# Kernel optimization log

Hardware: AMD Instinct MI355X
Metric: run time of the kernel (lower is better)

## Reference

```python
import jax, jax.numpy as jnp
import numpy as np

# static config (matches init_kwargs)
B, H, W, C = 8, 64, 64, 512
HEADS, WS, SHIFT = 16, 8, 4
N = WS * WS
HIDDEN = 4 * C
HEAD_DIM = C // HEADS
SCALE = HEAD_DIM ** -0.5
EPS = 1e-3  # keras LayerNormalization default epsilon


def _rel_pos_index(ws):
    # replicates tf.meshgrid default 'xy' indexing used in the source
    coords = np.stack(np.meshgrid(np.arange(ws), np.arange(ws)))  # [2, ws, ws]
    cf = coords.reshape(2, -1)
    rel = (cf[:, :, None] - cf[:, None, :]).transpose(1, 2, 0)  # [N, N, 2]
    rel[:, :, 0] += ws - 1
    rel[:, :, 1] += ws - 1
    rel[:, :, 0] *= 2 * ws - 1
    return jnp.asarray(rel.sum(-1))  # [N, N] int


def _attn_mask(h, w, ws, shift):
    img = np.zeros((h, w), dtype=np.float32)
    cnt = 0
    for hs in (slice(0, -ws), slice(-ws, -shift), slice(-shift, None)):
        for wsl in (slice(0, -ws), slice(-ws, -shift), slice(-shift, None)):
            img[hs, wsl] = cnt
            cnt += 1
    mw = img.reshape(h // ws, ws, w // ws, ws).transpose(0, 2, 1, 3).reshape(-1, ws * ws)  # [nW, N]
    diff = mw[:, None, :] - mw[:, :, None]
    return jnp.asarray(np.where(diff != 0, -100.0, 0.0).astype(np.float32))  # [nW, N, N]


REL_IDX = _rel_pos_index(WS)
ATTN_MASK = _attn_mask(H, W, WS, SHIFT)
NW = (H // WS) * (W // WS)


def _ln(x, g, b):
    mu = jnp.mean(x, -1, keepdims=True)
    var = jnp.mean(jnp.square(x - mu), -1, keepdims=True)
    return (x - mu) * jax.lax.rsqrt(var + EPS) * g + b


def setup_inputs() -> dict:
    key = jax.random.key(0)
    ks = jax.random.split(key, 14)
    s = 0.02
    return {
        "x": jax.random.normal(ks[0], (B, H * W, C), jnp.float32),
        "norm1_g": jnp.ones((C,), jnp.float32),
        "norm1_b": jnp.zeros((C,), jnp.float32),
        "qkv_w": jax.random.normal(ks[1], (C, 3 * C), jnp.float32) * s,
        "qkv_b": jnp.zeros((3 * C,), jnp.float32),
        "rpb_table": jax.random.normal(ks[2], ((2 * WS - 1) ** 2, HEADS), jnp.float32) * s,
        "proj_w": jax.random.normal(ks[3], (C, C), jnp.float32) * s,
        "proj_b": jnp.zeros((C,), jnp.float32),
        "norm2_g": jnp.ones((C,), jnp.float32),
        "norm2_b": jnp.zeros((C,), jnp.float32),
        "fc1_w": jax.random.normal(ks[4], (C, HIDDEN), jnp.float32) * s,
        "fc1_b": jnp.zeros((HIDDEN,), jnp.float32),
        "fc2_w": jax.random.normal(ks[5], (HIDDEN, C), jnp.float32) * s,
        "fc2_b": jnp.zeros((C,), jnp.float32),
    }


def reference(x, norm1_g, norm1_b, qkv_w, qkv_b, rpb_table, proj_w, proj_b,
              norm2_g, norm2_b, fc1_w, fc1_b, fc2_w, fc2_b):
    shortcut = x
    h = _ln(x, norm1_g, norm1_b).reshape(B, H, W, C)
    # cyclic shift (SW-MSA)
    h = jnp.roll(h, (-SHIFT, -SHIFT), axis=(1, 2))
    # window partition -> (B*nW, N, C)
    h = h.reshape(B, H // WS, WS, W // WS, WS, C).transpose(0, 1, 3, 2, 4, 5)
    h = h.reshape(B * NW, N, C)
    # qkv
    qkv = (h @ qkv_w + qkv_b).reshape(B * NW, N, 3, HEADS, HEAD_DIM).transpose(2, 0, 3, 1, 4)
    q, k, v = qkv[0] * SCALE, qkv[1], qkv[2]  # each [Bw, heads, N, hd]
    attn = jnp.einsum('bhnd,bhmd->bhnm', q, k)  # [Bw, heads, N, N]
    bias = rpb_table[REL_IDX.reshape(-1)].reshape(N, N, HEADS).transpose(2, 0, 1)
    attn = attn + bias[None]
    # shifted-window mask, per source: mask add -> softmax -> softmax AGAIN (source quirk)
    attn = attn.reshape(B, NW, HEADS, N, N) + ATTN_MASK[None, :, None]
    attn = attn.reshape(B * NW, HEADS, N, N)
    attn = jax.nn.softmax(attn, axis=-1)
    attn = jax.nn.softmax(attn, axis=-1)
    o = jnp.einsum('bhnm,bhmd->bhnd', attn, v).transpose(0, 2, 1, 3).reshape(B * NW, N, C)
    o = o @ proj_w + proj_b
    # window reverse + reverse shift
    o = o.reshape(B, H // WS, W // WS, WS, WS, C).transpose(0, 1, 3, 2, 4, 5).reshape(B, H, W, C)
    o = jnp.roll(o, (SHIFT, SHIFT), axis=(1, 2)).reshape(B, H * W, C)
    x = shortcut + o
    # MLP: source applies gelu twice (Dense activation + explicit gelu)
    y = _ln(x, norm2_g, norm2_b)
    y = jax.nn.gelu(jax.nn.gelu(y @ fc1_w + fc1_b, approximate=False), approximate=False)
    y = y @ fc2_w + fc2_b
    return x + y
```

## Files before the change

kernel.cpp:

```cpp
#include <hip/hip_runtime.h>
#include <hip/hip_bf16.h>
#include <math.h>


typedef unsigned short ushort_t;
typedef __attribute__((ext_vector_type(8))) short short8;
typedef __attribute__((ext_vector_type(8))) __bf16 bf16x8;
typedef __attribute__((ext_vector_type(4))) float f32x4;

#define DEVINL __device__ __forceinline__

DEVINL float bf2f(ushort_t u){ union {unsigned int i; float f;} c; c.i = ((unsigned)u)<<16; return c.f; }
DEVINL ushort_t f2bf(float f){ union {unsigned int i; float f;} c; c.f = f; unsigned r = c.i + 0x7fffu + ((c.i>>16)&1u); return (ushort_t)(r>>16); }

typedef const __attribute__((address_space(1))) void* gas_t;
typedef __attribute__((address_space(3))) void* las_t;
DEVINL void load_lds16(const void* g, void* l) {
  __builtin_amdgcn_global_load_lds((gas_t)g, (las_t)l, 16, 0, 0);
}

DEVINL float gelu_fast(float v){
  float z  = fabsf(v) * 0.70710678118654752f;
  float t  = __builtin_amdgcn_rcpf(fmaf(0.47047f, z, 1.0f));
  float p  = t * fmaf(t, fmaf(t, 0.7478556f, -0.0958798f), 0.3480242f);
  float e  = __expf(-z*z);
  float er = fmaf(-p, e, 1.0f);
  float hs = (v >= 0.f) ? 0.5f : -0.5f;
  return v * fmaf(hs, er, 0.5f);
}

DEVINL int win_map_row(int t){
  int bw = t >> 6, n = t & 63;
  int b  = bw >> 6, wdx = bw & 63;
  int wh = wdx >> 3, ww = wdx & 7;
  int r  = n >> 3,  c  = n & 7;
  int hh = (wh*8 + r + 4) & 63;
  int w2 = (ww*8 + c + 4) & 63;
  return (b << 12) + (hh << 6) + w2;
}

DEVINL void remap_mn(int bid, int nwg, int nbn, int BM, int BN, int& m0, int& n0){
  int q    = nwg >> 3;
  int lbid = (bid & 7)*q + (bid >> 3);
  m0 = (lbid / nbn) * BM;
  n0 = (lbid % nbn) * BN;
}

__global__ void transpose_all(const float* __restrict__ qkv_w, const float* __restrict__ proj_w,
                              const float* __restrict__ fc1_w, const float* __restrict__ fc2_w,
                              ushort_t* __restrict__ wqT, ushort_t* __restrict__ wpT,
                              ushort_t* __restrict__ w1T, ushort_t* __restrict__ w2T){
  __shared__ float t[32][33];
  int bid = blockIdx.x;
  const float* in; ushort_t* out; int R, Ccols, bx, by;
  if (bid < 768)      { in=qkv_w;  out=wqT; R=512;  Ccols=1536; bx=(bid%48)*32;        by=(bid/48)*32; }
  else if (bid < 1024){ int b=bid-768;  in=proj_w; out=wpT; R=512;  Ccols=512;  bx=(b%16)*32; by=(b/16)*32; }
  else if (bid < 2048){ int b=bid-1024; in=fc1_w;  out=w1T; R=512;  Ccols=2048; bx=(b%64)*32; by=(b/64)*32; }
  else                { int b=bid-2048; in=fc2_w;  out=w2T; R=2048; Ccols=512;  bx=(b%16)*32; by=(b/16)*32; }
  int x = threadIdx.x, y = threadIdx.y;
  #pragma unroll
  for (int i=0;i<32;i+=8) t[y+i][x] = in[(size_t)(by+y+i)*Ccols + bx + x];
  __syncthreads();
  #pragma unroll
  for (int i=0;i<32;i+=8) out[(size_t)(bx+y+i)*R + by + x] = f2bf(t[x][y+i]);
}

__global__ __launch_bounds__(256) void ln_kernel(const float* __restrict__ in,
    const float* __restrict__ g, const float* __restrict__ bta,
    ushort_t* __restrict__ out, int windowed){
  int tid = threadIdx.x; int l = tid & 63; int w = tid >> 6;
  int t = blockIdx.x * 4 + w;
  int src = windowed ? win_map_row(t) : t;
  const float* row = in + (size_t)src * 512;
  float4 v0 = *(const float4*)(row + l*8);
  float4 v1 = *(const float4*)(row + l*8 + 4);
  float f[8] = {v0.x,v0.y,v0.z,v0.w, v1.x,v1.y,v1.z,v1.w};
  float s=0.f, s2=0.f;
  #pragma unroll
  for (int j=0;j<8;j++){ s += f[j]; s2 += f[j]*f[j]; }
  #pragma unroll
  for (int m=1;m<64;m<<=1){ s += __shfl_xor(s,m); s2 += __shfl_xor(s2,m); }
  float mu  = s * (1.f/512.f);
  float var = s2*(1.f/512.f) - mu*mu;
  float rs  = rsqrtf(var + 1e-3f);
  float4 g0 = *(const float4*)(g + l*8),   g1 = *(const float4*)(g + l*8 + 4);
  float4 b0 = *(const float4*)(bta + l*8), b1 = *(const float4*)(bta + l*8 + 4);
  float gg[8] = {g0.x,g0.y,g0.z,g0.w, g1.x,g1.y,g1.z,g1.w};
  float bb[8] = {b0.x,b0.y,b0.z,b0.w, b1.x,b1.y,b1.z,b1.w};
  short8 o;
  #pragma unroll
  for (int j=0;j<8;j++) o[j] = (short)f2bf((f[j]-mu)*rs*gg[j] + bb[j]);
  *(short8*)(out + (size_t)t*512 + l*8) = o;
}

template<int EPI>
__global__ __launch_bounds__(512, 4) void gemmv(
    const ushort_t* __restrict__ A, const ushort_t* __restrict__ Bt,
    const float* __restrict__ bias, void* __restrict__ Cout_v,
    const float* __restrict__ xres, int M, int N, int K, int nbn)
{
  __shared__ ushort_t lds[24576];
  __shared__ float2 g2tab[(EPI==1)?1024:1];
  const int tid = threadIdx.x; const int l = tid & 63; const int w = tid >> 6;
  const int wm = w >> 1, wn = w & 1;
  int m0, n0; remap_mn(blockIdx.x, gridDim.x, nbn, 256, 128, m0, n0);
  const int lr = l & 15, lk = l >> 4;
  const int nt = K >> 5;

  if (EPI == 1){
    #pragma unroll
    for (int i=0;i<2;i++){
      int idx = tid*2 + i;
      float vi = -4.f + (float)idx*(1.f/128.f);
      float a  = gelu_fast(gelu_fast(vi));
      float b  = gelu_fast(gelu_fast(vi + (1.f/128.f)));
      g2tab[idx] = make_float2(a, b - a);
    }
  }

  const int r0 = tid >> 2;
  const int kc = ((tid & 3) - (r0 >> 1)) & 3;
  const size_t aG = (size_t)(m0 + r0) * K + kc*8;
  const size_t bG = (size_t)(n0 + r0) * K + kc*8;

  #define STAGE_T(tt, LB) do { \
    load_lds16(A  + aG +                  (size_t)(tt)*32, &lds[(LB) +        w*512]); \
    load_lds16(A  + aG + 128*(size_t)K +  (size_t)(tt)*32, &lds[(LB) + 4096 + w*512]); \
    load_lds16(Bt + bG +                  (size_t)(tt)*32, &lds[(LB) + 8192 + w*512]); \
  } while(0)

  int aoff[4], boff[4];
  #pragma unroll
  for (int mf=0; mf<4; mf++){
    int row = wm*64 + mf*16 + lr;
    aoff[mf] = (row*4 + ((lk + (row>>1)) & 3))*8;
  }
  #pragma unroll
  for (int nf=0; nf<4; nf++){
    int row = wn*64 + nf*16 + lr;
    boff[nf] = 8192 + (row*4 + ((lk + (row>>1)) & 3))*8;
  }

  f32x4 acc[4][4] = {};

  STAGE_T(0, 0);
  STAGE_T(1, 12288);
  asm volatile("s_waitcnt vmcnt(3)" ::: "memory");
  __builtin_amdgcn_s_barrier();

  for (int t = 0; t < nt; ++t){
    const int Lb = (t & 1) ? 12288 : 0;
    const int t2 = (t+2 < nt) ? t+2 : nt-1;
    bf16x8 af[4], bfr[4];
    #pragma unroll
    for (int mf=0; mf<4; mf++) af[mf]  = *(const bf16x8*)&lds[Lb + aoff[mf]];
    #pragma unroll
    for (int nf=0; nf<4; nf++) bfr[nf] = *(const bf16x8*)&lds[Lb + boff[nf]];
    __builtin_amdgcn_sched_barrier(0);
    asm volatile("s_waitcnt lgkmcnt(0)" ::: "memory");
    __builtin_amdgcn_s_barrier();
    __builtin_amdgcn_sched_barrier(0);
    STAGE_T(t2, Lb);
    __builtin_amdgcn_sched_barrier(0);
    __builtin_amdgcn_s_setprio(1);
    #pragma unroll
    for (int mf=0; mf<4; mf++)
      #pragma unroll
      for (int nf=0; nf<4; nf++)
        acc[mf][nf] = __builtin_amdgcn_mfma_f32_16x16x32_bf16(af[mf], bfr[nf], acc[mf][nf], 0,0,0);
    __builtin_amdgcn_s_setprio(0);
    __builtin_amdgcn_sched_barrier(0);
    asm volatile("s_waitcnt vmcnt(3)" ::: "memory");
    __builtin_amdgcn_s_barrier();
  }

  asm volatile("s_waitcnt vmcnt(0)" ::: "memory");
  __builtin_amdgcn_s_barrier();
  __builtin_amdgcn_sched_barrier(0);

  int erow = l >> 2, ecc = l & 3;
  if (EPI == 0 || EPI == 1){
    ushort_t* tw = lds + w*1152;
    #pragma unroll
    for (int mf=0; mf<4; mf++){
      #pragma unroll
      for (int nf=0; nf<4; nf++){
        float bz = bias[n0 + wn*64 + nf*16 + lr];
        #pragma unroll
        for (int rg=0; rg<4; rg++){
          float v = acc[mf][nf][rg] + bz;
          if (EPI == 1){
            float u  = fminf(fmaxf((v + 4.f)*128.f, 0.f), 1023.999f);
            int   iu = (int)u;
            float fr = u - (float)iu;
            float2 pq = g2tab[iu];
            float rr = fmaf(fr, pq.y, pq.x);
            rr = (v >  4.f) ? v   : rr;
            v  = (v < -4.f) ? 0.f : rr;
          }
          tw[(lk*4+rg)*72 + nf*16 + lr] = f2bf(v);
        }
      }
      short8 p0 = *(const short8*)(tw + erow*72 + ecc*16);
      short8 p1 = *(const short8*)(tw + erow*72 + ecc*16 + 8);
      int grow = m0 + wm*64 + mf*16 + erow;
      int col  = n0 + wn*64 + ecc*16;
      *(short8*)&((ushort_t*)Cout_v)[(size_t)grow*N + col]     = p0;
      *(short8*)&((ushort_t*)Cout_v)[(size_t)grow*N + col + 8] = p1;
    }
  } else {
    float* twf = (float*)lds + w*1152;
    #pragma unroll
    for (int mf=0; mf<4; mf++){
      #pragma unroll
      for (int nf=0; nf<4; nf++){
        float bz = bias[n0 + wn*64 + nf*16 + lr];
        #pragma unroll
        for (int rg=0; rg<4; rg++)
          twf[(lk*4+rg)*72 + nf*16 + lr] = acc[mf][nf][rg] + bz;
      }
      int grow = m0 + wm*64 + mf*16 + erow;
      int col  = n0 + wn*64 + ecc*16;
      float4 q0 = *(const float4*)(twf + erow*72 + ecc*16);
      float4 q1 = *(const float4*)(twf + erow*72 + ecc*16 + 4);
      float4 q2 = *(const float4*)(twf + erow*72 + ecc*16 + 8);
      float4 q3 = *(const float4*)(twf + erow*72 + ecc*16 + 12);
      size_t off;
      float* o = (float*)Cout_v;
      if (EPI == 2){
        int row2 = win_map_row(grow);
        off = (size_t)row2*512 + col;
        float4 x0 = *(const float4*)(xres + off);
        float4 x1 = *(const float4*)(xres + off + 4);
        float4 x2 = *(const float4*)(xres + off + 8);
        float4 x3 = *(const float4*)(xres + off + 12);
        q0 = make_float4(q0.x+x0.x, q0.y+x0.y, q0.z+x0.z, q0.w+x0.w);
        q1 = make_float4(q1.x+x1.x, q1.y+x1.y, q1.z+x1.z, q1.w+x1.w);
        q2 = make_float4(q2.x+x2.x, q2.y+x2.y, q2.z+x2.z, q2.w+x2.w);
        q3 = make_float4(q3.x+x3.x, q3.y+x3.y, q3.z+x3.z, q3.w+x3.w);
      } else {
        off = (size_t)grow*N + col;
        float4 x0 = *(const float4*)(o + off);
        float4 x1 = *(const float4*)(o + off + 4);
        float4 x2 = *(const float4*)(o + off + 8);
        float4 x3 = *(const float4*)(o + off + 12);
        q0 = make_float4(q0.x+x0.x, q0.y+x0.y, q0.z+x0.z, q0.w+x0.w);
        q1 = make_float4(q1.x+x1.x, q1.y+x1.y, q1.z+x1.z, q1.w+x1.w);
        q2 = make_float4(q2.x+x2.x, q2.y+x2.y, q2.z+x2.z, q2.w+x2.w);
        q3 = make_float4(q3.x+x3.x, q3.y+x3.y, q3.z+x3.z, q3.w+x3.w);
      }
      *(float4*)(o + off)      = q0;
      *(float4*)(o + off + 4)  = q1;
      *(float4*)(o + off + 8)  = q2;
      *(float4*)(o + off + 12) = q3;
    }
  }
  #undef STAGE_T
}

DEVINL int band3(int t){ return (t<56) ? 0 : ((t<60) ? 1 : 2); }

union frag_u { short8 s; bf16x8 b; };

__global__ __launch_bounds__(256) void attn_kernel(const ushort_t* __restrict__ qkv,
    const float* __restrict__ rpb, ushort_t* __restrict__ o)
{
  __shared__ ushort_t sP[4][64*64];
  __shared__ ushort_t sV[4][64*32];
  int tid = threadIdx.x; int l = tid & 63; int w = tid >> 6;
  int p = blockIdx.x*4 + w;
  int bw = p >> 4, head = p & 15;
  int lr = l & 15, lk = l >> 4;
  const ushort_t* base = qkv + (size_t)bw*64*1536 + head*32;

  #pragma unroll
  for (int c=0;c<4;c++){
    int idx = c*64 + l;
    int row = idx >> 2, cc = idx & 3;
    load_lds16(base + 1024 + (size_t)row*1536 + cc*8, &sV[w][0] + c*512);
  }

  bf16x8 qf[4], kf[4];
  #pragma unroll
  for (int m=0;m<4;m++) qf[m] = *(const bf16x8*)(base +       (size_t)(m*16+lr)*1536 + lk*8);
  #pragma unroll
  for (int m=0;m<4;m++) kf[m] = *(const bf16x8*)(base + 512 + (size_t)(m*16+lr)*1536 + lk*8);

  f32x4 s[4][4] = {};
  #pragma unroll
  for (int m=0;m<4;m++)
    #pragma unroll
    for (int n=0;n<4;n++)
      s[m][n] = __builtin_amdgcn_mfma_f32_16x16x32_bf16(qf[m], kf[n], s[m][n], 0,0,0);

  int wdx = bw & 63; int wh = wdx >> 3, ww = wdx & 7;
  const float SCALE = 0.17677669529663687f;
  #pragma unroll
  for (int m=0;m<4;m++){
    #pragma unroll
    for (int r=0;r<4;r++){
      int i  = m*16 + lk*4 + r;
      int ri = band3(wh*8 + (i>>3))*3 + band3(ww*8 + (i&7));
      int ix = i & 7, iy = i >> 3;
      #pragma unroll
      for (int n=0;n<4;n++){
        int j   = n*16 + lr;
        int rj  = band3(wh*8 + (j>>3))*3 + band3(ww*8 + (j&7));
        int idx = 15*(ix - (j&7) + 7) + (iy - (j>>3) + 7);
        float bv = rpb[idx*16 + head];
        float mk = (ri == rj) ? 0.f : -100.f;
        s[m][n][r] = s[m][n][r]*SCALE + bv + mk;
      }
    }
  }

  #pragma unroll
  for (int pass=0; pass<2; pass++){
    #pragma unroll
    for (int m=0;m<4;m++){
      #pragma unroll
      for (int r=0;r<4;r++){
        float mx = fmaxf(fmaxf(s[m][0][r], s[m][1][r]), fmaxf(s[m][2][r], s[m][3][r]));
        #pragma unroll
        for (int d=1;d<16;d<<=1) mx = fmaxf(mx, __shfl_xor(mx, d));
        float sum = 0.f;
        #pragma unroll
        for (int n=0;n<4;n++){ float e = __expf(s[m][n][r]-mx); s[m][n][r]=e; sum += e; }
        #pragma unroll
        for (int d=1;d<16;d<<=1) sum += __shfl_xor(sum, d);
        float inv = 1.f/sum;
        #pragma unroll
        for (int n=0;n<4;n++) s[m][n][r] = s[m][n][r]*inv;
      }
    }
  }

  ushort_t* pl = &sP[w][0];
  #pragma unroll
  for (int m=0;m<4;m++)
    #pragma unroll
    for (int r=0;r<4;r++){
      int i = m*16 + lk*4 + r;
      #pragma unroll
      for (int n=0;n<4;n++){
        int j = n*16 + lr;
        int byte = i*128 + ((j*2) ^ ((i&7)<<4));
        pl[byte>>1] = f2bf(s[m][n][r]);
      }
    }

  asm volatile("s_waitcnt vmcnt(0)" ::: "memory");
  const ushort_t* vl = &sV[w][0];
  frag_u vf[2][2];
  #pragma unroll
  for (int kb=0;kb<2;kb++)
    #pragma unroll
    for (int nb=0;nb<2;nb++){
      #pragma unroll
      for (int j=0;j<8;j++){
        int k = kb*32 + lk*8 + j;
        vf[kb][nb].s[j] = (short)vl[k*32 + nb*16 + lr];
      }
    }

  f32x4 oacc[4][2] = {};
  #pragma unroll
  for (int m=0;m<4;m++){
    #pragma unroll
    for (int kb=0;kb<2;kb++){
      int row  = m*16 + lr;
      int byte = row*128 + ((kb*64 + lk*16) ^ ((row&7)<<4));
      bf16x8 pf = *(const bf16x8*)(pl + (byte>>1));
      #pragma unroll
      for (int nb=0;nb<2;nb++)
        oacc[m][nb] = __builtin_amdgcn_mfma_f32_16x16x32_bf16(pf, vf[kb][nb].b, oacc[m][nb], 0,0,0);
    }
  }

  ushort_t* orow = o + (size_t)bw*64*512 + head*32;
  #pragma unroll
  for (int m=0;m<4;m++)
    #pragma unroll
    for (int nb=0;nb<2;nb++)
      #pragma unroll
      for (int r=0;r<4;r++){
        int i = m*16 + lk*4 + r;
        int d = nb*16 + lr;
        orow[(size_t)i*512 + d] = f2bf(oacc[m][nb][r]);
      }
}

extern "C" void kernel_launch(void* const* d_in, const int* in_sizes, int n_in,
                              void* d_out, int out_size, void* d_ws, size_t ws_size,
                              hipStream_t stream) {
  const float* x      = (const float*)d_in[0];
  const float* n1g    = (const float*)d_in[1];
  const float* n1b    = (const float*)d_in[2];
  const float* qkv_w  = (const float*)d_in[3];
  const float* qkv_b  = (const float*)d_in[4];
  const float* rpb    = (const float*)d_in[5];
  const float* proj_w = (const float*)d_in[6];
  const float* proj_b = (const float*)d_in[7];
  const float* n2g    = (const float*)d_in[8];
  const float* n2b    = (const float*)d_in[9];
  const float* fc1_w  = (const float*)d_in[10];
  const float* fc1_b  = (const float*)d_in[11];
  const float* fc2_w  = (const float*)d_in[12];
  const float* fc2_b  = (const float*)d_in[13];
  float* out = (float*)d_out;

  ushort_t* ws = (ushort_t*)d_ws;
  size_t off = 0;
  ushort_t* wqT = ws + off; off += (size_t)1536*512;
  ushort_t* wpT = ws + off; off += (size_t)512*512;
  ushort_t* w1T = ws + off; off += (size_t)2048*512;
  ushort_t* w2T = ws + off; off += (size_t)512*2048;
  ushort_t* R1  = ws + off; off += (size_t)32768*512;
  ushort_t* R2  = ws + off; off += (size_t)32768*2048;
  if (ws_size < off*sizeof(ushort_t)) return;

  transpose_all<<<3072, dim3(32,8), 0, stream>>>(qkv_w, proj_w, fc1_w, fc2_w, wqT, wpT, w1T, w2T);

  ln_kernel<<<8192, 256, 0, stream>>>(x, n1g, n1b, R1, 1);
  gemmv<0><<<1536, 512, 0, stream>>>(R1, wqT, qkv_b, R2, nullptr, 32768, 1536, 512, 12);
  attn_kernel<<<2048, 256, 0, stream>>>(R2, rpb, R1);
  gemmv<2><<<512, 512, 0, stream>>>(R1, wpT, proj_b, out, x, 32768, 512, 512, 4);
  ln_kernel<<<8192, 256, 0, stream>>>(out, n2g, n2b, R1, 0);
  gemmv<1><<<2048, 512, 0, stream>>>(R1, w1T, fc1_b, R2, nullptr, 32768, 2048, 512, 16);
  gemmv<3><<<512, 512, 0, stream>>>(R2, w2T, fc2_b, out, nullptr, 32768, 512, 2048, 4);
}
```

Before: 407.4 us.

## Add 256x256-tile GEMM with BK=64 phased pipeline for QKV, proj, fc2

Adds a gemm256 kernel using 256x256 output tiles, a K-step of 64, 64KB LDS double buffering and a four-phase schedule that interleaves A/B staging with MFMA groups. QKV, projection and fc2 GEMMs now use it, which raises arithmetic intensity and halves the tile count. The fc1 GEMM keeps the old kernel, but its double-GELU table changes from interpolated 1024 entries to nearest-lookup 2048 entries, trading accuracy for fewer epilogue ops. The larger tile cuts occupancy to 2 blocks per CU and leaves only 256 blocks for the N=512 GEMMs, which may underfill the GPU.

```diff
diff --git a/kernel.cpp b/kernel.cpp
--- a/kernel.cpp
+++ b/kernel.cpp
@@ -9,6 +9,8 @@
 typedef __attribute__((ext_vector_type(4))) float f32x4;
 
 #define DEVINL __device__ __forceinline__
+
+union frag_u { short8 s; bf16x8 b; };
 
 DEVINL float bf2f(ushort_t u){ union {unsigned int i; float f;} c; c.i = ((unsigned)u)<<16; return c.f; }
 DEVINL ushort_t f2bf(float f){ union {unsigned int i; float f;} c; c.f = f; unsigned r = c.i + 0x7fffu + ((c.i>>16)&1u); return (ushort_t)(r>>16); }
@@ -93,117 +95,118 @@
   *(short8*)(out + (size_t)t*512 + l*8) = o;
 }
 
+#define G_STAGE(G, base, h, tt, LB) do { \
+    load_lds16((G) + (base) + (size_t)((h)*128)*K    + (size_t)(tt)*64, &lds[(LB) + (h)*8192 +        w*512]); \
+    load_lds16((G) + (base) + (size_t)((h)*128+64)*K + (size_t)(tt)*64, &lds[(LB) + (h)*8192 + 4096 + w*512]); \
+  } while(0)
+
+#define NOWAIT
+#define VM4 asm volatile("s_waitcnt vmcnt(4)" ::: "memory")
+
+#define PHASE(mp, STAGE_STMT, EXTRA) do { \
+    bf16x8 a0 = *(const bf16x8*)&lds[ALb + aoff[2*(mp)  ][0]]; \
+    bf16x8 a1 = *(const bf16x8*)&lds[ALb + aoff[2*(mp)  ][1]]; \
+    bf16x8 a2 = *(const bf16x8*)&lds[ALb + aoff[2*(mp)+1][0]]; \
+    bf16x8 a3 = *(const bf16x8*)&lds[ALb + aoff[2*(mp)+1][1]]; \
+    STAGE_STMT; \
+    EXTRA; \
+    __builtin_amdgcn_s_barrier(); \
+    asm volatile("s_waitcnt lgkmcnt(0)" ::: "memory"); \
+    __builtin_amdgcn_sched_barrier(0); \
+    __builtin_amdgcn_s_setprio(1); \
+    _Pragma("unroll") \
+    for (int nf=0; nf<4; nf++){ \
+      acc[2*(mp)  ][nf] = __builtin_amdgcn_mfma_f32_16x16x32_bf16(a0, bfr[nf][0], acc[2*(mp)  ][nf], 0,0,0); \
+      acc[2*(mp)  ][nf] = __builtin_amdgcn_mfma_f32_16x16x32_bf16(a1, bfr[nf][1], acc[2*(mp)  ][nf], 0,0,0); \
+      acc[2*(mp)+1][nf] = __builtin_amdgcn_mfma_f32_16x16x32_bf16(a2, bfr[nf][0], acc[2*(mp)+1][nf], 0,0,0); \
+      acc[2*(mp)+1][nf] = __builtin_amdgcn_mfma_f32_16x16x32_bf16(a3, bfr[nf][1], acc[2*(mp)+1][nf], 0,0,0); \
+    } \
+    __builtin_amdgcn_s_setprio(0); \
+    __builtin_amdgcn_sched_barrier(0); \
+    __builtin_amdgcn_s_barrier(); \
+  } while(0)
+
 template<int EPI>
-__global__ __launch_bounds__(512, 4) void gemmv(
+__global__ __launch_bounds__(512, 2) void gemm256(
     const ushort_t* __restrict__ A, const ushort_t* __restrict__ Bt,
     const float* __restrict__ bias, void* __restrict__ Cout_v,
     const float* __restrict__ xres, int M, int N, int K, int nbn)
 {
-  __shared__ ushort_t lds[24576];
-  __shared__ float2 g2tab[(EPI==1)?1024:1];
+  __shared__ ushort_t lds[65536];
   const int tid = threadIdx.x; const int l = tid & 63; const int w = tid >> 6;
-  const int wm = w >> 1, wn = w & 1;
-  int m0, n0; remap_mn(blockIdx.x, gridDim.x, nbn, 256, 128, m0, n0);
+  const int wm = w >> 2, wn = w & 3;
+  int m0, n0;
+  remap_mn(blockIdx.x, gridDim.x, nbn, 256, 256, m0, n0);
   const int lr = l & 15, lk = l >> 4;
-  const int nt = K >> 5;
-
-  if (EPI == 1){
-    #pragma unroll
-    for (int i=0;i<2;i++){
-      int idx = tid*2 + i;
-      float vi = -4.f + (float)idx*(1.f/128.f);
-      float a  = gelu_fast(gelu_fast(vi));
-      float b  = gelu_fast(gelu_fast(vi + (1.f/128.f)));
-      g2tab[idx] = make_float2(a, b - a);
-    }
-  }
-
-  const int r0 = tid >> 2;
-  const int kc = ((tid & 3) - (r0 >> 1)) & 3;
-  const size_t aG = (size_t)(m0 + r0) * K + kc*8;
-  const size_t bG = (size_t)(n0 + r0) * K + kc*8;
-
-  #define STAGE_T(tt, LB) do { \
-    load_lds16(A  + aG +                  (size_t)(tt)*32, &lds[(LB) +        w*512]); \
-    load_lds16(A  + aG + 128*(size_t)K +  (size_t)(tt)*32, &lds[(LB) + 4096 + w*512]); \
-    load_lds16(Bt + bG +                  (size_t)(tt)*32, &lds[(LB) + 8192 + w*512]); \
-  } while(0)
-
-  int aoff[4], boff[4];
-  #pragma unroll
-  for (int mf=0; mf<4; mf++){
-    int row = wm*64 + mf*16 + lr;
-    aoff[mf] = (row*4 + ((lk + (row>>1)) & 3))*8;
+  const int nt = K >> 6;
+
+  const int r0 = tid >> 3;
+  const int kc = ((tid & 7) - r0) & 7;
+  const size_t aRow0 = (size_t)(m0 + r0) * K + kc * 8;
+  const size_t bRow0 = (size_t)(n0 + r0) * K + kc * 8;
+
+  int aoff[8][2], boff[4][2];
+  #pragma unroll
+  for (int mf=0; mf<8; mf++){
+    int row = wm*128 + mf*16 + lr;
+    #pragma unroll
+    for (int kh=0; kh<2; kh++){ int c = kh*4 + lk; aoff[mf][kh] = (row*8 + ((c + row)&7))*8; }
   }
   #pragma unroll
   for (int nf=0; nf<4; nf++){
     int row = wn*64 + nf*16 + lr;
-    boff[nf] = 8192 + (row*4 + ((lk + (row>>1)) & 3))*8;
-  }
-
-  f32x4 acc[4][4] = {};
-
-  STAGE_T(0, 0);
-  STAGE_T(1, 12288);
-  asm volatile("s_waitcnt vmcnt(3)" ::: "memory");
+    #pragma unroll
+    for (int kh=0; kh<2; kh++){ int c = kh*4 + lk; boff[nf][kh] = (row*8 + ((c + row)&7))*8; }
+  }
+
+  f32x4 acc[8][4] = {};
+
+  G_STAGE(A,  aRow0, 0, 0, 0);
+  G_STAGE(A,  aRow0, 1, 0, 0);
+  G_STAGE(Bt, bRow0, 0, 0, 16384);
+  G_STAGE(Bt, bRow0, 1, 0, 16384);
+  G_STAGE(Bt, bRow0, 0, 1, 32768+16384);
+  G_STAGE(Bt, bRow0, 1, 1, 32768+16384);
+  VM4;
   __builtin_amdgcn_s_barrier();
 
-  for (int t = 0; t < nt; ++t){
-    const int Lb = (t & 1) ? 12288 : 0;
-    const int t2 = (t+2 < nt) ? t+2 : nt-1;
-    bf16x8 af[4], bfr[4];
-    #pragma unroll
-    for (int mf=0; mf<4; mf++) af[mf]  = *(const bf16x8*)&lds[Lb + aoff[mf]];
-    #pragma unroll
-    for (int nf=0; nf<4; nf++) bfr[nf] = *(const bf16x8*)&lds[Lb + boff[nf]];
-    __builtin_amdgcn_sched_barrier(0);
-    asm volatile("s_waitcnt lgkmcnt(0)" ::: "memory");
-    __builtin_amdgcn_s_barrier();
-    __builtin_amdgcn_sched_barrier(0);
-    STAGE_T(t2, Lb);
-    __builtin_amdgcn_sched_barrier(0);
-    __builtin_amdgcn_s_setprio(1);
-    #pragma unroll
-    for (int mf=0; mf<4; mf++)
-      #pragma unroll
-      for (int nf=0; nf<4; nf++)
-        acc[mf][nf] = __builtin_amdgcn_mfma_f32_16x16x32_bf16(af[mf], bfr[nf], acc[mf][nf], 0,0,0);
-    __builtin_amdgcn_s_setprio(0);
-    __builtin_amdgcn_sched_barrier(0);
-    asm volatile("s_waitcnt vmcnt(3)" ::: "memory");
-    __builtin_amdgcn_s_barrier();
+  for (int t = 0; t < nt; ++t) {
+    const int b   = t & 1;
+    const int ALb = b*32768, BLb = ALb + 16384;
+    const int ALn = (b^1)*32768;
+    const int t1  = (t+1 < nt) ? t+1 : t;
+    const int t2  = (t+2 < nt) ? t+2 : t;
+
+    bf16x8 bfr[4][2];
+    #pragma unroll
+    for (int nf=0; nf<4; nf++){
+      bfr[nf][0] = *(const bf16x8*)&lds[BLb + boff[nf][0]];
+      bfr[nf][1] = *(const bf16x8*)&lds[BLb + boff[nf][1]];
+    }
+    PHASE(0, G_STAGE(A,  aRow0, 0, t1, ALn), NOWAIT);
+    PHASE(1, G_STAGE(A,  aRow0, 1, t1, ALn), NOWAIT);
+    PHASE(2, G_STAGE(Bt, bRow0, 0, t2, BLb), NOWAIT);
+    PHASE(3, G_STAGE(Bt, bRow0, 1, t2, BLb), VM4);
   }
 
   asm volatile("s_waitcnt vmcnt(0)" ::: "memory");
   __builtin_amdgcn_s_barrier();
-  __builtin_amdgcn_sched_barrier(0);
 
   int erow = l >> 2, ecc = l & 3;
-  if (EPI == 0 || EPI == 1){
+  if (EPI == 0){
     ushort_t* tw = lds + w*1152;
     #pragma unroll
-    for (int mf=0; mf<4; mf++){
+    for (int mf=0; mf<8; mf++){
       #pragma unroll
       for (int nf=0; nf<4; nf++){
         float bz = bias[n0 + wn*64 + nf*16 + lr];
         #pragma unroll
-        for (int rg=0; rg<4; rg++){
-          float v = acc[mf][nf][rg] + bz;
-          if (EPI == 1){
-            float u  = fminf(fmaxf((v + 4.f)*128.f, 0.f), 1023.999f);
-            int   iu = (int)u;
-            float fr = u - (float)iu;
-            float2 pq = g2tab[iu];
-            float rr = fmaf(fr, pq.y, pq.x);
-            rr = (v >  4.f) ? v   : rr;
-            v  = (v < -4.f) ? 0.f : rr;
-          }
-          tw[(lk*4+rg)*72 + nf*16 + lr] = f2bf(v);
-        }
+        for (int rg=0; rg<4; rg++)
+          tw[(lk*4+rg)*72 + nf*16 + lr] = f2bf(acc[mf][nf][rg] + bz);
       }
       short8 p0 = *(const short8*)(tw + erow*72 + ecc*16);
       short8 p1 = *(const short8*)(tw + erow*72 + ecc*16 + 8);
-      int grow = m0 + wm*64 + mf*16 + erow;
+      int grow = m0 + wm*128 + mf*16 + erow;
       int col  = n0 + wn*64 + ecc*16;
       *(short8*)&((ushort_t*)Cout_v)[(size_t)grow*N + col]     = p0;
       *(short8*)&((ushort_t*)Cout_v)[(size_t)grow*N + col + 8] = p1;
@@ -211,7 +214,7 @@
   } else {
     float* twf = (float*)lds + w*1152;
     #pragma unroll
-    for (int mf=0; mf<4; mf++){
+    for (int mf=0; mf<8; mf++){
       #pragma unroll
       for (int nf=0; nf<4; nf++){
         float bz = bias[n0 + wn*64 + nf*16 + lr];
@@ -219,14 +222,13 @@
         for (int rg=0; rg<4; rg++)
           twf[(lk*4+rg)*72 + nf*16 + lr] = acc[mf][nf][rg] + bz;
       }
-      int grow = m0 + wm*64 + mf*16 + erow;
+      int grow = m0 + wm*128 + mf*16 + erow;
       int col  = n0 + wn*64 + ecc*16;
       float4 q0 = *(const float4*)(twf + erow*72 + ecc*16);
       float4 q1 = *(const float4*)(twf + erow*72 + ecc*16 + 4);
       float4 q2 = *(const float4*)(twf + erow*72 + ecc*16 + 8);
       float4 q3 = *(const float4*)(twf + erow*72 + ecc*16 + 12);
       size_t off;
-      float* o = (float*)Cout_v;
       if (EPI == 2){
         int row2 = win_map_row(grow);
         off = (size_t)row2*512 + col;
@@ -240,6 +242,7 @@
         q3 = make_float4(q3.x+x3.x, q3.y+x3.y, q3.z+x3.z, q3.w+x3.w);
       } else {
         off = (size_t)grow*N + col;
+        float* o = (float*)Cout_v;
         float4 x0 = *(const float4*)(o + off);
         float4 x1 = *(const float4*)(o + off + 4);
         float4 x2 = *(const float4*)(o + off + 8);
@@ -249,18 +252,128 @@
         q2 = make_float4(q2.x+x2.x, q2.y+x2.y, q2.z+x2.z, q2.w+x2.w);
         q3 = make_float4(q3.x+x3.x, q3.y+x3.y, q3.z+x3.z, q3.w+x3.w);
       }
+      float* o = (float*)Cout_v;
       *(float4*)(o + off)      = q0;
       *(float4*)(o + off + 4)  = q1;
       *(float4*)(o + off + 8)  = q2;
       *(float4*)(o + off + 12) = q3;
     }
   }
+}
+
+template<int EPI>
+__global__ __launch_bounds__(512, 4) void gemmv(
+    const ushort_t* __restrict__ A, const ushort_t* __restrict__ Bt,
+    const float* __restrict__ bias, void* __restrict__ Cout_v,
+    const float* __restrict__ xres, int M, int N, int K, int nbn)
+{
+  __shared__ ushort_t lds[24576];
+  __shared__ float g2tab[(EPI==1)?2048:1];
+  const int tid = threadIdx.x; const int l = tid & 63; const int w = tid >> 6;
+  const int wm = w >> 1, wn = w & 1;
+  int m0, n0; remap_mn(blockIdx.x, gridDim.x, nbn, 256, 128, m0, n0);
+  const int lr = l & 15, lk = l >> 4;
+  const int nt = K >> 5;
+
+  if (EPI == 1){
+    #pragma unroll
+    for (int i=0;i<4;i++){
+      int idx = tid*4 + i;
+      float vi = -4.f + (float)idx*(1.f/256.f);
+      g2tab[idx] = gelu_fast(gelu_fast(vi));
+    }
+  }
+
+  const int r0 = tid >> 2;
+  const int kc = ((tid & 3) - (r0 >> 1)) & 3;
+  const size_t aG = (size_t)(m0 + r0) * K + kc*8;
+  const size_t bG = (size_t)(n0 + r0) * K + kc*8;
+
+  #define STAGE_T(tt, LB) do { \
+    load_lds16(A  + aG +                  (size_t)(tt)*32, &lds[(LB) +        w*512]); \
+    load_lds16(A  + aG + 128*(size_t)K +  (size_t)(tt)*32, &lds[(LB) + 4096 + w*512]); \
+    load_lds16(Bt + bG +                  (size_t)(tt)*32, &lds[(LB) + 8192 + w*512]); \
+  } while(0)
+
+  int aoff[4], boff[4];
+  #pragma unroll
+  for (int mf=0; mf<4; mf++){
+    int row = wm*64 + mf*16 + lr;
+    aoff[mf] = (row*4 + ((lk + (row>>1)) & 3))*8;
+  }
+  #pragma unroll
+  for (int nf=0; nf<4; nf++){
+    int row = wn*64 + nf*16 + lr;
+    boff[nf] = 8192 + (row*4 + ((lk + (row>>1)) & 3))*8;
+  }
+
+  f32x4 acc[4][4] = {};
+
+  STAGE_T(0, 0);
+  STAGE_T(1, 12288);
+  asm volatile("s_waitcnt vmcnt(3)" ::: "memory");
+  __builtin_amdgcn_s_barrier();
+
+  for (int t = 0; t < nt; ++t){
+    const int Lb = (t & 1) ? 12288 : 0;
+    const int t2 = (t+2 < nt) ? t+2 : nt-1;
+    bf16x8 af[4], bfr[4];
+    #pragma unroll
+    for (int mf=0; mf<4; mf++) af[mf]  = *(const bf16x8*)&lds[Lb + aoff[mf]];
+    #pragma unroll
+    for (int nf=0; nf<4; nf++) bfr[nf] = *(const bf16x8*)&lds[Lb + boff[nf]];
+    __builtin_amdgcn_sched_barrier(0);
+    asm volatile("s_waitcnt lgkmcnt(0)" ::: "memory");
+    __builtin_amdgcn_s_barrier();
+    __builtin_amdgcn_sched_barrier(0);
+    STAGE_T(t2, Lb);
+    __builtin_amdgcn_sched_barrier(0);
+    __builtin_amdgcn_s_setprio(1);
+    #pragma unroll
+    for (int mf=0; mf<4; mf++)
+      #pragma unroll
+      for (int nf=0; nf<4; nf++)
+        acc[mf][nf] = __builtin_amdgcn_mfma_f32_16x16x32_bf16(af[mf], bfr[nf], acc[mf][nf], 0,0,0);
+    __builtin_amdgcn_s_setprio(0);
+    __builtin_amdgcn_sched_barrier(0);
+    asm volatile("s_waitcnt vmcnt(3)" ::: "memory");
+    __builtin_amdgcn_s_barrier();
+  }
+
+  asm volatile("s_waitcnt vmcnt(0)" ::: "memory");
+  __builtin_amdgcn_s_barrier();
+  __builtin_amdgcn_sched_barrier(0);
+
+  int erow = l >> 2, ecc = l & 3;
+  ushort_t* tw = lds + w*1152;
+  #pragma unroll
+  for (int mf=0; mf<4; mf++){
+    #pragma unroll
+    for (int nf=0; nf<4; nf++){
+      float bz = bias[n0 + wn*64 + nf*16 + lr];
+      #pragma unroll
+      for (int rg=0; rg<4; rg++){
+        float v = acc[mf][nf][rg] + bz;
+        if (EPI == 1){
+          float u  = fminf(fmaxf(fmaf(v, 256.f, 1024.5f), 0.f), 2047.f);
+          float rr = g2tab[(int)u];
+          rr = (v >  4.f) ? v   : rr;
+          v  = (v < -4.f) ? 0.f : rr;
+        }
+        tw[(lk*4+rg)*72 + nf*16 + lr] = f2bf(v);
+      }
+    }
+    short8 p0 = *(const short8*)(tw + erow*72 + ecc*16);
+    short8 p1 = *(const short8*)(tw + erow*72 + ecc*16 + 8);
+    int grow = m0 + wm*64 + mf*16 + erow;
+    int col  = n0 + wn*64 + ecc*16;
+    *(short8*)&((ushort_t*)Cout_v)[(size_t)grow*N + col]     = p0;
+    *(short8*)&((ushort_t*)Cout_v)[(size_t)grow*N + col + 8] = p1;
+  }
   #undef STAGE_T
 }
 
 DEVINL int band3(int t){ return (t<56) ? 0 : ((t<60) ? 1 : 2); }
-
-union frag_u { short8 s; bf16x8 b; };
 
 __global__ __launch_bounds__(256) void attn_kernel(const ushort_t* __restrict__ qkv,
     const float* __restrict__ rpb, ushort_t* __restrict__ o)
@@ -422,10 +535,10 @@
   transpose_all<<<3072, dim3(32,8), 0, stream>>>(qkv_w, proj_w, fc1_w, fc2_w, wqT, wpT, w1T, w2T);
 
   ln_kernel<<<8192, 256, 0, stream>>>(x, n1g, n1b, R1, 1);
-  gemmv<0><<<1536, 512, 0, stream>>>(R1, wqT, qkv_b, R2, nullptr, 32768, 1536, 512, 12);
+  gemm256<0><<<768, 512, 0, stream>>>(R1, wqT, qkv_b, R2, nullptr, 32768, 1536, 512, 6);
   attn_kernel<<<2048, 256, 0, stream>>>(R2, rpb, R1);
-  gemmv<2><<<512, 512, 0, stream>>>(R1, wpT, proj_b, out, x, 32768, 512, 512, 4);
+  gemm256<2><<<256, 512, 0, stream>>>(R1, wpT, proj_b, out, x, 32768, 512, 512, 2);
   ln_kernel<<<8192, 256, 0, stream>>>(out, n2g, n2b, R1, 0);
   gemmv<1><<<2048, 512, 0, stream>>>(R1, w1T, fc1_b, R2, nullptr, 32768, 2048, 512, 16);
-  gemmv<3><<<512, 512, 0, stream>>>(R2, w2T, fc2_b, out, nullptr, 32768, 512, 2048, 4);
-}
+  gemm256<3><<<256, 512, 0, stream>>>(R2, w2T, fc2_b, out, nullptr, 32768, 512, 2048, 2);
+}
```

Result: faster. 389.5 us (-4.4%).
